# Optimization experiments

Hardware: AMD Instinct MI355X
Metric: run time of the kernel (lower is better)

The kernel has to match this reference:

```python
import jax, jax.numpy as jnp
import numpy as np

D_MODEL, D_STATE, D_CONV, EXPAND = 1024, 16, 4, 2
D_INNER = EXPAND * D_MODEL  # 2048
DT_RANK = (D_MODEL + 15) // 16  # 64
B, L = 2, 2048


def setup_inputs() -> dict:
    key = jax.random.key(0)
    ks = jax.random.split(key, 10)
    x = jax.random.normal(ks[0], (B, L, D_MODEL), dtype=jnp.float32)
    # Linear weights (torch convention: (out, in)); Mamba uses bias=False for in/out proj
    in_proj_w = jax.random.normal(ks[1], (2 * D_INNER, D_MODEL), dtype=jnp.float32) / np.sqrt(D_MODEL)
    conv_w = jax.random.normal(ks[2], (D_INNER, 1, D_CONV), dtype=jnp.float32) / np.sqrt(D_CONV)
    conv_b = jax.random.normal(ks[3], (D_INNER,), dtype=jnp.float32) * 0.02
    x_proj_w = jax.random.normal(ks[4], (DT_RANK + 2 * D_STATE, D_INNER), dtype=jnp.float32) / np.sqrt(D_INNER)
    dt_proj_w = jax.random.normal(ks[5], (D_INNER, DT_RANK), dtype=jnp.float32) * (DT_RANK ** -0.5)
    # dt bias init so softplus(bias) in [dt_min, dt_max]
    dt_min, dt_max = 1e-3, 1e-1
    u = jax.random.uniform(ks[6], (D_INNER,), dtype=jnp.float32)
    dt = jnp.exp(u * (np.log(dt_max) - np.log(dt_min)) + np.log(dt_min))
    dt_proj_b = dt + jnp.log(-jnp.expm1(-dt))  # inverse softplus
    # S4D-real init: A = -(1..d_state)
    A_log = jnp.log(jnp.tile(jnp.arange(1, D_STATE + 1, dtype=jnp.float32), (D_INNER, 1)))
    D_skip = jnp.ones((D_INNER,), dtype=jnp.float32)
    out_proj_w = jax.random.normal(ks[7], (D_MODEL, D_INNER), dtype=jnp.float32) / np.sqrt(D_INNER)
    return {"x": x, "in_proj_w": in_proj_w, "conv_w": conv_w, "conv_b": conv_b,
            "x_proj_w": x_proj_w, "dt_proj_w": dt_proj_w, "dt_proj_b": dt_proj_b,
            "A_log": A_log, "D_skip": D_skip, "out_proj_w": out_proj_w}


def _mamba_forward(x, in_proj_w, conv_w, conv_b, x_proj_w, dt_proj_w, dt_proj_b, A_log, D_skip, out_proj_w):
    Bsz, Lseq, _ = x.shape
    xz = jnp.einsum('bld,ed->ble', x, in_proj_w)          # (B, L, 2*d_inner)
    x_in, z = jnp.split(xz, 2, axis=-1)                    # each (B, L, d_inner)
    # depthwise causal conv1d (left pad d_conv-1)
    xc = jnp.transpose(x_in, (0, 2, 1))                    # (B, d_inner, L)
    xc = jax.lax.conv_general_dilated(
        xc, conv_w, window_strides=(1,), padding=[(D_CONV - 1, 0)],
        dimension_numbers=('NCH', 'OIH', 'NCH'), feature_group_count=D_INNER)
    xc = xc + conv_b[None, :, None]
    x_act = jax.nn.silu(jnp.transpose(xc, (0, 2, 1)))      # (B, L, d_inner)
    # input-dependent SSM parameters
    x_dbl = jnp.einsum('bld,ed->ble', x_act, x_proj_w)     # (B, L, dt_rank+2*d_state)
    dt_low, Bm, Cm = jnp.split(x_dbl, [DT_RANK, DT_RANK + D_STATE], axis=-1)
    delta = jax.nn.softplus(jnp.einsum('blr,dr->bld', dt_low, dt_proj_w) + dt_proj_b)  # (B,L,d)
    A = -jnp.exp(A_log)                                    # (d_inner, d_state)

    def step(h, inp):
        d_t, B_t, C_t, u_t = inp                           # (B,d),(B,N),(B,N),(B,d)
        dA = jnp.exp(d_t[..., None] * A)                   # (B,d,N)
        dBu = (d_t * u_t)[..., None] * B_t[:, None, :]     # (B,d,N)
        h = dA * h + dBu
        y = jnp.einsum('bdn,bn->bd', h, C_t)
        return h, y

    h0 = jnp.zeros((Bsz, D_INNER, D_STATE), dtype=x.dtype)
    xs = (jnp.swapaxes(delta, 0, 1), jnp.swapaxes(Bm, 0, 1),
          jnp.swapaxes(Cm, 0, 1), jnp.swapaxes(x_act, 0, 1))
    _, ys = jax.lax.scan(step, h0, xs)                     # ys: (L, B, d_inner)
    y = jnp.swapaxes(ys, 0, 1) + x_act * D_skip            # skip connection
    y = y * jax.nn.silu(z)                                 # gate
    return jnp.einsum('bld,ed->ble', y, out_proj_w)        # (B, L, d_model)


def reference(x, in_proj_w, conv_w, conv_b, x_proj_w, dt_proj_w, dt_proj_b, A_log, D_skip, out_proj_w):
    return _mamba_forward(x, in_proj_w, conv_w, conv_b, x_proj_w, dt_proj_w, dt_proj_b, A_log, D_skip, out_proj_w)
```

## Files before the change

kernel.cpp:

```cpp
#include <hip/hip_runtime.h>
#include <hip/hip_bf16.h>
#include <cstdint>

#define D_STATE 16
#define D_INNER 2048
#define DT_RANK 64
#define SEQ 2048
#define BL 4096
#define NCHUNK 128
#define CHUNK 16
#define XP_N 96
#define XP_KS 8
#define LOG2E 1.44269504088896340736f

typedef short bf16x8 __attribute__((ext_vector_type(8)));
typedef short short8 __attribute__((ext_vector_type(8)));
typedef float f32x4 __attribute__((ext_vector_type(4)));

__device__ __forceinline__ float siluf(float x) {
  return __fdividef(x, 1.f + __expf(-x));
}

__device__ __forceinline__ float softplusf(float v) {
  return fmaxf(v, 0.f) + __logf(1.f + __expf(-fabsf(v)));
}

__device__ __forceinline__ float exp2fast(float x) {
  return __builtin_amdgcn_exp2f(x);
}

__device__ __forceinline__ unsigned short f2bf_bits(float x) {
  __hip_bfloat16 h = __float2bfloat16(x);
  return *reinterpret_cast<unsigned short*>(&h);
}

__device__ __forceinline__ float bf2f(unsigned short u) {
  return __int_as_float(((unsigned int)u) << 16);
}

__device__ __forceinline__ void gload_lds16(const void* g, void* l) {
  __builtin_amdgcn_global_load_lds((const __attribute__((address_space(1))) unsigned int*)g,
                                   (__attribute__((address_space(3))) unsigned int*)l,
                                   16, 0, 0);
}

#define BARRIER() asm volatile("s_barrier" ::: "memory")
#define VMCNT(n)  asm volatile("s_waitcnt vmcnt(" #n ")" ::: "memory")

__global__ __launch_bounds__(256) void f2bf_multi(const float* __restrict__ x, __hip_bfloat16* __restrict__ x_bf,
                                                  const float* __restrict__ inw, __hip_bfloat16* __restrict__ inw_bf,
                                                  const float* __restrict__ xpw, __hip_bfloat16* __restrict__ wpad,
                                                  const float* __restrict__ dtw, __hip_bfloat16* __restrict__ dtw_bf,
                                                  const float* __restrict__ outw, __hip_bfloat16* __restrict__ outw_bf) {
  const int blk = blockIdx.x;
  const float* src;
  __hip_bfloat16* dst;
  int base;
  if (blk < 2048)      { src = x;    dst = x_bf;    base = blk; }
  else if (blk < 4096) { src = inw;  dst = inw_bf;  base = blk - 2048; }
  else if (blk < 4192) { src = xpw;  dst = wpad;    base = blk - 4096; }
  else if (blk < 4256) { src = dtw;  dst = dtw_bf;  base = blk - 4192; }
  else                 { src = outw; dst = outw_bf; base = blk - 4256; }
  const int i = (base * 256 + threadIdx.x) * 8;
  float4 v0 = *reinterpret_cast<const float4*>(&src[i]);
  float4 v1 = *reinterpret_cast<const float4*>(&src[i + 4]);
  short8 r;
  r[0] = f2bf_bits(v0.x); r[1] = f2bf_bits(v0.y); r[2] = f2bf_bits(v0.z); r[3] = f2bf_bits(v0.w);
  r[4] = f2bf_bits(v1.x); r[5] = f2bf_bits(v1.y); r[6] = f2bf_bits(v1.z); r[7] = f2bf_bits(v1.w);
  *reinterpret_cast<short8*>(&dst[i]) = r;
}

__global__ __launch_bounds__(256) void dtlow_bf_kernel(const float* __restrict__ x_dbl,
                                                       __hip_bfloat16* __restrict__ dtlow_bf) {
  const int i = blockIdx.x * 256 + threadIdx.x;
  const int row = i >> 3;
  const int c8 = (i & 7) * 8;
  float4 v0 = *reinterpret_cast<const float4*>(&x_dbl[(size_t)row * 96 + c8]);
  float4 v1 = *reinterpret_cast<const float4*>(&x_dbl[(size_t)row * 96 + c8 + 4]);
  short8 r;
  r[0] = f2bf_bits(v0.x); r[1] = f2bf_bits(v0.y); r[2] = f2bf_bits(v0.z); r[3] = f2bf_bits(v0.w);
  r[4] = f2bf_bits(v1.x); r[5] = f2bf_bits(v1.y); r[6] = f2bf_bits(v1.z); r[7] = f2bf_bits(v1.w);
  *reinterpret_cast<short8*>(&dtlow_bf[(size_t)row * 64 + c8]) = r;
}

template <typename OutT>
__global__ __launch_bounds__(512, 1) void gemm256_8ph(const __hip_bfloat16* __restrict__ A,
                                                      const __hip_bfloat16* __restrict__ B,
                                                      OutT* __restrict__ C,
                                                      int K, int lda, int ldb, int ldc) {
  __shared__ __align__(16) unsigned short lds[65536];
  const int tid = threadIdx.x;
  const int wv = tid >> 6, lane = tid & 63;
  const int wr = wv >> 2, wc = wv & 3;
  const int m0 = blockIdx.y * 256, n0 = blockIdx.x * 256;
  const int frow = lane & 15;
  const int fu = lane >> 4;
  const int rsw = frow & 7;
  const int sr = lane >> 3;
  const int su = (lane & 7) ^ sr;

  const unsigned short* Ag = (const unsigned short*)A;
  const unsigned short* Bg = (const unsigned short*)B;

  f32x4 acc[8][4];
#pragma unroll
  for (int i = 0; i < 8; ++i)
#pragma unroll
    for (int j = 0; j < 4; ++j) acc[i][j] = {0.f, 0.f, 0.f, 0.f};

  auto stageA = [&](int buf, int g, int kg) {
    const int rowb = g * 64 + wv * 8;
    gload_lds16(&Ag[(size_t)(m0 + rowb + sr) * lda + kg + su * 8],
                &lds[buf * 32768 + rowb * 64]);
  };
  auto stageB = [&](int buf, int g, int kg) {
    const int rowb = g * 64 + wv * 8;
    gload_lds16(&Bg[(size_t)(n0 + rowb + sr) * ldb + kg + su * 8],
                &lds[buf * 32768 + 16384 + rowb * 64]);
  };
  auto fragA = [&](int buf, int mi, int kk) -> bf16x8 {
    const int row = wr * 128 + mi * 16 + frow;
    return *reinterpret_cast<const bf16x8*>(
        &lds[buf * 32768 + row * 64 + (((kk << 2) | fu) ^ rsw) * 8]);
  };
  auto fragB = [&](int buf, int ni, int kk) -> bf16x8 {
    const int row = wc * 64 + ni * 16 + frow;
    return *reinterpret_cast<const bf16x8*>(
        &lds[buf * 32768 + 16384 + row * 64 + (((kk << 2) | fu) ^ rsw) * 8]);
  };

#define QUAD(MB)                                                                        \
  _Pragma("unroll")                                                                     \
  for (int mi = 0; mi < 4; ++mi)                                                        \
    _Pragma("unroll")                                                                   \
    for (int ni = 0; ni < 4; ++ni)                                                      \
      acc[MB + mi][ni] =                                                                \
          __builtin_amdgcn_mfma_f32_16x16x32_bf16(af[mi], bfr[ni], acc[MB + mi][ni], 0, 0, 0);

  stageB(0, 0, 0); stageB(0, 1, 0); stageB(0, 2, 0); stageB(0, 3, 0);
  stageA(0, 0, 0); stageA(0, 2, 0); stageA(0, 1, 0); stageA(0, 3, 0);
  VMCNT(2);
  BARRIER();

  const int NT = K >> 6;
  int cur = 0;
  for (int t = 0; t < NT - 1; ++t) {
    const int nxt = cur ^ 1;
    const int kn = (t + 1) << 6;
    bf16x8 af[4], bfr[4];
#pragma unroll
    for (int mi = 0; mi < 4; ++mi) af[mi] = fragA(cur, mi, 0);
#pragma unroll
    for (int ni = 0; ni < 4; ++ni) bfr[ni] = fragB(cur, ni, 0);
    stageB(nxt, 0, kn); stageB(nxt, 1, kn);
    VMCNT(2);
    BARRIER();
    __builtin_amdgcn_s_setprio(1);
    QUAD(0);
    __builtin_amdgcn_s_setprio(0);
    BARRIER();
#pragma unroll
    for (int mi = 0; mi < 4; ++mi) af[mi] = fragA(cur, 4 + mi, 0);
    stageB(nxt, 2, kn); stageB(nxt, 3, kn);
    BARRIER();
    __builtin_amdgcn_s_setprio(1);
    QUAD(4);
    __builtin_amdgcn_s_setprio(0);
    BARRIER();
#pragma unroll
    for (int mi = 0; mi < 4; ++mi) af[mi] = fragA(cur, mi, 1);
#pragma unroll
    for (int ni = 0; ni < 4; ++ni) bfr[ni] = fragB(cur, ni, 1);
    stageA(nxt, 0, kn); stageA(nxt, 2, kn);
    BARRIER();
    __builtin_amdgcn_s_setprio(1);
    QUAD(0);
    __builtin_amdgcn_s_setprio(0);
    BARRIER();
#pragma unroll
    for (int mi = 0; mi < 4; ++mi) af[mi] = fragA(cur, 4 + mi, 1);
    stageA(nxt, 1, kn); stageA(nxt, 3, kn);
    VMCNT(2);
    BARRIER();
    __builtin_amdgcn_s_setprio(1);
    QUAD(4);
    __builtin_amdgcn_s_setprio(0);
    BARRIER();
    cur = nxt;
  }
  {
    bf16x8 af[4], bfr[4];
#pragma unroll
    for (int mi = 0; mi < 4; ++mi) af[mi] = fragA(cur, mi, 0);
#pragma unroll
    for (int ni = 0; ni < 4; ++ni) bfr[ni] = fragB(cur, ni, 0);
    VMCNT(0);
    BARRIER();
    __builtin_amdgcn_s_setprio(1);
    QUAD(0);
    __builtin_amdgcn_s_setprio(0);
    BARRIER();
#pragma unroll
    for (int mi = 0; mi < 4; ++mi) af[mi] = fragA(cur, 4 + mi, 0);
    BARRIER();
    __builtin_amdgcn_s_setprio(1);
    QUAD(4);
    __builtin_amdgcn_s_setprio(0);
    BARRIER();
#pragma unroll
    for (int mi = 0; mi < 4; ++mi) af[mi] = fragA(cur, mi, 1);
#pragma unroll
    for (int ni = 0; ni < 4; ++ni) bfr[ni] = fragB(cur, ni, 1);
    BARRIER();
    __builtin_amdgcn_s_setprio(1);
    QUAD(0);
    __builtin_amdgcn_s_setprio(0);
    BARRIER();
#pragma unroll
    for (int mi = 0; mi < 4; ++mi) af[mi] = fragA(cur, 4 + mi, 1);
    __builtin_amdgcn_s_setprio(1);
    QUAD(4);
    __builtin_amdgcn_s_setprio(0);
  }
#undef QUAD

  const int crow = fu * 4;
  const int ccol = frow;
#pragma unroll
  for (int mi = 0; mi < 8; ++mi)
#pragma unroll
    for (int ni = 0; ni < 4; ++ni) {
      const int gcol = n0 + wc * 64 + ni * 16 + ccol;
#pragma unroll
      for (int j = 0; j < 4; ++j) {
        const int grow = m0 + wr * 128 + mi * 16 + crow + j;
        if constexpr (sizeof(OutT) == 2) {
          C[(size_t)grow * ldc + gcol] = __float2bfloat16(acc[mi][ni][j]);
        } else {
          C[(size_t)grow * ldc + gcol] = acc[mi][ni][j];
        }
      }
    }
}

template <int BM, int BN>
__device__ __forceinline__ void stage_tiles(const unsigned short* __restrict__ Ag,
                                            const unsigned short* __restrict__ Bg,
                                            unsigned short* buf, int m0, int n0, int k0,
                                            int lda, int ldb, int sr, int sk, int wv) {
#pragma unroll
  for (int g = 0; g < BM / 64; ++g)
    gload_lds16(&Ag[(size_t)(m0 + g * 64 + sr) * lda + k0 + sk], &buf[g * 2048 + wv * 512]);
#pragma unroll
  for (int g = 0; g < BN / 64; ++g)
    gload_lds16(&Bg[(size_t)(n0 + g * 64 + sr) * ldb + k0 + sk], &buf[BM * 32 + g * 2048 + wv * 512]);
}

template <int BM, int BN, int NSTORE, bool SPLITK, typename OutT>
__global__ __launch_bounds__(256) void gemm_bt(const __hip_bfloat16* __restrict__ A,
                                               const __hip_bfloat16* __restrict__ B,
                                               OutT* __restrict__ C,
                                               int K, int lda, int ldb, int ldc) {
  constexpr int WM = BM / 2, WN = BN / 2;
  constexpr int MI = WM / 16, NI = WN / 16;
  constexpr int BUFS = (BM + BN) * 32;
  __shared__ __align__(16) unsigned short lds[2 * BUFS];
  const int tid = threadIdx.x;
  const int wv = tid >> 6, lane = tid & 63;
  const int wr = wv >> 1, wc = wv & 1;
  const int m0 = blockIdx.y * BM;
  int n0, koff;
  if constexpr (SPLITK) {
    n0 = 0;
    koff = blockIdx.x * K;
    C += (size_t)blockIdx.x * BL * NSTORE;
  } else {
    n0 = blockIdx.x * BN;
    koff = 0;
  }
  const int sr = tid >> 2;
  const int sk = (tid & 3) * 8;
  const int frow = lane & 15;
  const int fk = (lane >> 4) * 8;

  f32x4 acc[MI][NI];
#pragma unroll
  for (int i = 0; i < MI; ++i)
#pragma unroll
    for (int j = 0; j < NI; ++j) acc[i][j] = {0.f, 0.f, 0.f, 0.f};

  const unsigned short* Ag = (const unsigned short*)A;
  const unsigned short* Bg = (const unsigned short*)B;

  stage_tiles<BM, BN>(Ag, Bg, &lds[0], m0, n0, koff, lda, ldb, sr, sk, wv);
  __syncthreads();
  int sel = 0;
  for (int k0 = 0; k0 < K; k0 += 32) {
    if (k0 + 32 < K)
      stage_tiles<BM, BN>(Ag, Bg, &lds[(sel ^ 1) * BUFS], m0, n0, koff + k0 + 32, lda, ldb, sr, sk, wv);
    const unsigned short* Abuf = &lds[sel * BUFS];
    const unsigned short* Bbuf = &lds[sel * BUFS + BM * 32];
    bf16x8 af[MI], bfr[NI];
#pragma unroll
    for (int mi = 0; mi < MI; ++mi)
      af[mi] = *reinterpret_cast<const bf16x8*>(&Abuf[(wr * WM + mi * 16 + frow) * 32 + fk]);
#pragma unroll
    for (int ni = 0; ni < NI; ++ni)
      bfr[ni] = *reinterpret_cast<const bf16x8*>(&Bbuf[(wc * WN + ni * 16 + frow) * 32 + fk]);
#pragma unroll
    for (int mi = 0; mi < MI; ++mi)
#pragma unroll
      for (int ni = 0; ni < NI; ++ni)
        acc[mi][ni] = __builtin_amdgcn_mfma_f32_16x16x32_bf16(af[mi], bfr[ni], acc[mi][ni], 0, 0, 0);
    __syncthreads();
    sel ^= 1;
  }

  const int crow = (lane >> 4) * 4;
  const int ccol = lane & 15;
#pragma unroll
  for (int mi = 0; mi < MI; ++mi)
#pragma unroll
    for (int ni = 0; ni < NI; ++ni) {
      const int gcol = n0 + wc * WN + ni * 16 + ccol;
      if constexpr (NSTORE < BN) {
        if (gcol >= NSTORE) continue;
      }
#pragma unroll
      for (int j = 0; j < 4; ++j) {
        const int grow = m0 + wr * WM + mi * 16 + crow + j;
        if constexpr (sizeof(OutT) == 2) {
          C[(size_t)grow * ldc + gcol] = __float2bfloat16(acc[mi][ni][j]);
        } else {
          C[(size_t)grow * ldc + gcol] = acc[mi][ni][j];
        }
      }
    }
}

__global__ __launch_bounds__(256) void xproj_reduce(const float* __restrict__ Cpart,
                                                    float* __restrict__ x_dbl) {
  const int i = blockIdx.x * 256 + threadIdx.x;
  float s = 0.f;
#pragma unroll
  for (int z = 0; z < XP_KS; ++z) s += Cpart[(size_t)z * BL * XP_N + i];
  x_dbl[i] = s;
}

__global__ __launch_bounds__(256) void conv_silu_kernel(const __hip_bfloat16* __restrict__ xz_bf,
                                                        const float* __restrict__ conv_w,
                                                        const float* __restrict__ conv_b,
                                                        __hip_bfloat16* __restrict__ x_act_bf) {
  const int idx = blockIdx.x * 256 + threadIdx.x;
  const int d8 = (idx << 3) & (D_INNER - 1);
  const int bl = idx >> 8;
  const int l = bl & (SEQ - 1);

  float acc[8];
  {
    float4 cb0 = *reinterpret_cast<const float4*>(&conv_b[d8]);
    float4 cb1 = *reinterpret_cast<const float4*>(&conv_b[d8 + 4]);
    acc[0] = cb0.x; acc[1] = cb0.y; acc[2] = cb0.z; acc[3] = cb0.w;
    acc[4] = cb1.x; acc[5] = cb1.y; acc[6] = cb1.z; acc[7] = cb1.w;
  }
  float4 cw[8];
#pragma unroll
  for (int j = 0; j < 8; ++j)
    cw[j] = *reinterpret_cast<const float4*>(&conv_w[(d8 + j) * 4]);

#pragma unroll
  for (int k = 0; k < 4; ++k) {
    if (l + k - 3 >= 0) {
      short8 v = *reinterpret_cast<const short8*>(&xz_bf[(size_t)(bl + k - 3) * 4096 + d8]);
      const float w0[8] = {cw[0].x, cw[1].x, cw[2].x, cw[3].x, cw[4].x, cw[5].x, cw[6].x, cw[7].x};
      const float w1[8] = {cw[0].y, cw[1].y, cw[2].y, cw[3].y, cw[4].y, cw[5].y, cw[6].y, cw[7].y};
      const float w2[8] = {cw[0].z, cw[1].z, cw[2].z, cw[3].z, cw[4].z, cw[5].z, cw[6].z, cw[7].z};
      const float w3[8] = {cw[0].w, cw[1].w, cw[2].w, cw[3].w, cw[4].w, cw[5].w, cw[6].w, cw[7].w};
      const float* wk = (k == 0) ? w0 : (k == 1) ? w1 : (k == 2) ? w2 : w3;
#pragma unroll
      for (int j = 0; j < 8; ++j) acc[j] = fmaf(bf2f((unsigned short)v[j]), wk[j], acc[j]);
    }
  }

  short8 ob;
#pragma unroll
  for (int j = 0; j < 8; ++j) ob[j] = f2bf_bits(siluf(acc[j]));
  *reinterpret_cast<short8*>(&x_act_bf[(size_t)bl * D_INNER + d8]) = ob;
}

__global__ __launch_bounds__(256) void scan_pass1(const __hip_bfloat16* __restrict__ delta_bf,
                                                  const __hip_bfloat16* __restrict__ x_act_bf,
                                                  const float* __restrict__ x_dbl,
                                                  const float* __restrict__ A_log,
                                                  const float* __restrict__ dt_proj_b,
                                                  float* __restrict__ chunkS,
                                                  __hip_bfloat16* __restrict__ chunkH) {
  const int blk = blockIdx.x;
  const int d = ((blk & 7) << 8) + threadIdx.x;
  const int c = (blk >> 3) & (NCHUNK - 1);
  const int b = blk >> 10;
  const int base = b * SEQ + c * CHUNK;

  float Av[16];
#pragma unroll
  for (int q = 0; q < 4; ++q) {
    float4 a = *reinterpret_cast<const float4*>(&A_log[d * 16 + q * 4]);
    Av[q * 4 + 0] = -__expf(a.x) * LOG2E; Av[q * 4 + 1] = -__expf(a.y) * LOG2E;
    Av[q * 4 + 2] = -__expf(a.z) * LOG2E; Av[q * 4 + 3] = -__expf(a.w) * LOG2E;
  }
  const float bias = dt_proj_b[d];

  const unsigned short* dp = (const unsigned short*)delta_bf + (size_t)base * D_INNER + d;
  const unsigned short* up = (const unsigned short*)x_act_bf + (size_t)base * D_INNER + d;
  const float* xb = x_dbl + (size_t)base * 96 + DT_RANK;

  float h[16];
#pragma unroll
  for (int n = 0; n < 16; ++n) h[n] = 0.f;
  float S = 0.f;

  float dv0 = bf2f(dp[0]), uv0 = bf2f(up[0]);
  float dv1 = bf2f(dp[D_INNER]), uv1 = bf2f(up[D_INNER]);
  dp += 2 * D_INNER; up += 2 * D_INNER;
  for (int l = 0; l < CHUNK; ++l) {
    const float dv2 = bf2f(*dp), uv2 = bf2f(*up);
    dp += D_INNER; up += D_INNER;

    const float dv = softplusf(dv0 + bias);
    S += dv;
    const float du = dv * uv0;
#pragma unroll
    for (int n = 0; n < 16; ++n) {
      const float dA = exp2fast(dv * Av[n]);
      h[n] = fmaf(dA, h[n], du * xb[n]);
    }
    xb += 96;
    dv0 = dv1; uv0 = uv1; dv1 = dv2; uv1 = uv2;
  }

  const size_t sidx = (size_t)(b * NCHUNK + c) * D_INNER + d;
  chunkS[sidx] = S;
  unsigned short* hp = (unsigned short*)chunkH + sidx * 16;
  short8 h0v, h1v;
#pragma unroll
  for (int n = 0; n < 8; ++n) { h0v[n] = f2bf_bits(h[n]); h1v[n] = f2bf_bits(h[8 + n]); }
  *reinterpret_cast<short8*>(hp) = h0v;
  *reinterpret_cast<short8*>(hp + 8) = h1v;
}

__global__ __launch_bounds__(256) void scan_pass2(const float* __restrict__ chunkS,
                                                  const float* __restrict__ A_log,
                                                  __hip_bfloat16* chunkH) {
  const int s = blockIdx.x * 256 + threadIdx.x;
  const int n = s & 15;
  const int d = (s >> 4) & (D_INNER - 1);
  const int b = s >> 15;
  const float Aval = -__expf(A_log[d * 16 + n]) * LOG2E;

  unsigned short* hb = (unsigned short*)chunkH;
  size_t sidx = (size_t)b * NCHUNK * D_INNER + d;
  float aS = chunkS[sidx];
  float hE = bf2f(hb[sidx * 16 + n]);
  float H = 0.f;
  for (int c = 0; c < NCHUNK; ++c) {
    const size_t sidx2 = sidx + D_INNER;
    const float naS = chunkS[sidx2];
    const float nhE = bf2f(hb[sidx2 * 16 + n]);
    const float aP = exp2fast(Aval * aS);
    hb[sidx * 16 + n] = f2bf_bits(H);
    H = fmaf(aP, H, hE);
    sidx = sidx2; aS = naS; hE = nhE;
  }
}

__global__ __launch_bounds__(256) void scan_pass3(const __hip_bfloat16* __restrict__ delta_bf,
                                                  const __hip_bfloat16* __restrict__ x_act_bf,
                                                  const float* __restrict__ x_dbl,
                                                  const float* __restrict__ A_log,
                                                  const float* __restrict__ dt_proj_b,
                                                  const __hip_bfloat16* __restrict__ chunkH0,
                                                  const float* __restrict__ D_skip,
                                                  __hip_bfloat16* xz_bf) {
  const int blk = blockIdx.x;
  const int d = ((blk & 7) << 8) + threadIdx.x;
  const int c = (blk >> 3) & (NCHUNK - 1);
  const int b = blk >> 10;
  const int base = b * SEQ + c * CHUNK;

  float Av[16];
#pragma unroll
  for (int q = 0; q < 4; ++q) {
    float4 a = *reinterpret_cast<const float4*>(&A_log[d * 16 + q * 4]);
    Av[q * 4 + 0] = -__expf(a.x) * LOG2E; Av[q * 4 + 1] = -__expf(a.y) * LOG2E;
    Av[q * 4 + 2] = -__expf(a.z) * LOG2E; Av[q * 4 + 3] = -__expf(a.w) * LOG2E;
  }
  const float bias = dt_proj_b[d];
  const float Dv = D_skip[d];

  const unsigned short* dp = (const unsigned short*)delta_bf + (size_t)base * D_INNER + d;
  const unsigned short* up = (const unsigned short*)x_act_bf + (size_t)base * D_INNER + d;
  const float* xb = x_dbl + (size_t)base * 96 + DT_RANK;
  const unsigned short* zr = (const unsigned short*)xz_bf + (size_t)base * 4096 + D_INNER + d;
  __hip_bfloat16* yp = xz_bf + (size_t)base * 4096 + d;

  float h[16];
  {
    const unsigned short* hp = (const unsigned short*)chunkH0 +
                               ((size_t)(b * NCHUNK + c) * D_INNER + d) * 16;
    short8 a8 = *reinterpret_cast<const short8*>(hp);
    short8 b8 = *reinterpret_cast<const short8*>(hp + 8);
#pragma unroll
    for (int n = 0; n < 8; ++n) {
      h[n] = bf2f((unsigned short)a8[n]);
      h[8 + n] = bf2f((unsigned short)b8[n]);
    }
  }

  float dv0 = bf2f(dp[0]), uv0 = bf2f(up[0]);
  float dv1 = bf2f(dp[D_INNER]), uv1 = bf2f(up[D_INNER]);
  dp += 2 * D_INNER; up += 2 * D_INNER;
  float zv = bf2f(zr[0]);
  zr += 4096;
  for (int l = 0; l < CHUNK; ++l) {
    const float dv2 = bf2f(*dp), uv2 = bf2f(*up);
    dp += D_INNER; up += D_INNER;
    const float nzv = bf2f(*zr);
    zr += 4096;

    const float dv = softplusf(dv0 + bias);
    const float du = dv * uv0;
    float p = 0.f;
#pragma unroll
    for (int n = 0; n < 16; ++n) {
      const float dA = exp2fast(dv * Av[n]);
      h[n] = fmaf(dA, h[n], du * xb[n]);
      p = fmaf(h[n], xb[16 + n], p);
    }
    xb += 96;
    const float yv = fmaf(uv0, Dv, p) * siluf(zv);
    yp[0] = __float2bfloat16(yv);
    yp += 4096;

    dv0 = dv1; uv0 = uv1; dv1 = dv2; uv1 = uv2; zv = nzv;
  }
}

extern "C" void kernel_launch(void* const* d_in, const int* in_sizes, int n_in,
                              void* d_out, int out_size, void* d_ws, size_t ws_size,
                              hipStream_t stream) {
  const float* x          = (const float*)d_in[0];
  const float* in_proj_w  = (const float*)d_in[1];
  const float* conv_w     = (const float*)d_in[2];
  const float* conv_b     = (const float*)d_in[3];
  const float* x_proj_w   = (const float*)d_in[4];
  const float* dt_proj_w  = (const float*)d_in[5];
  const float* dt_proj_b  = (const float*)d_in[6];
  const float* A_log      = (const float*)d_in[7];
  const float* D_skip     = (const float*)d_in[8];
  const float* out_proj_w = (const float*)d_in[9];
  float* out = (float*)d_out;

  char* ws = (char*)d_ws;
  __hip_bfloat16* xz_bf    = (__hip_bfloat16*)(ws);
  __hip_bfloat16* x_act_bf = (__hip_bfloat16*)(ws + 33554432);
  __hip_bfloat16* delta_bf = (__hip_bfloat16*)(ws + 50331648);
  __hip_bfloat16* x_bf     = (__hip_bfloat16*)(ws + 67108864);
  __hip_bfloat16* inw_bf   = (__hip_bfloat16*)(ws + 75497472);
  float* Cpart             = (float*)(ws + 67108864);
  float* x_dbl             = (float*)(ws + 100663296);
  __hip_bfloat16* chunkH   = (__hip_bfloat16*)(ws + 102236160);
  float* chunkS            = (float*)(ws + 135790592);
  __hip_bfloat16* wpad     = (__hip_bfloat16*)(ws + 137887744);
  __hip_bfloat16* dtlow_bf = (__hip_bfloat16*)(ws + 138412032);
  __hip_bfloat16* dtw_bf   = (__hip_bfloat16*)(ws + 138936320);
  __hip_bfloat16* outw_bf  = (__hip_bfloat16*)(ws + 139198464);

  f2bf_multi<<<5280, 256, 0, stream>>>(x, x_bf, in_proj_w, inw_bf, x_proj_w, wpad,
                                       dt_proj_w, dtw_bf, out_proj_w, outw_bf);

  gemm256_8ph<__hip_bfloat16><<<dim3(16, 16), 512, 0, stream>>>(
      x_bf, inw_bf, xz_bf, 1024, 1024, 1024, 4096);

  conv_silu_kernel<<<(BL * D_INNER) / 8 / 256, 256, 0, stream>>>(
      xz_bf, conv_w, conv_b, x_act_bf);

  gemm_bt<128, 128, XP_N, true, float><<<dim3(XP_KS, 32), 256, 0, stream>>>(
      x_act_bf, wpad, Cpart, 2048 / XP_KS, 2048, 2048, XP_N);
  xproj_reduce<<<(BL * XP_N) / 256, 256, 0, stream>>>(Cpart, x_dbl);

  dtlow_bf_kernel<<<128, 256, 0, stream>>>(x_dbl, dtlow_bf);
  gemm_bt<128, 128, 128, false, __hip_bfloat16><<<dim3(16, 32), 256, 0, stream>>>(
      dtlow_bf, dtw_bf, delta_bf, 64, 64, 64, 2048);

  scan_pass1<<<2048, 256, 0, stream>>>(delta_bf, x_act_bf, x_dbl, A_log, dt_proj_b,
                                       chunkS, chunkH);
  scan_pass2<<<256, 256, 0, stream>>>(chunkS, A_log, chunkH);
  scan_pass3<<<2048, 256, 0, stream>>>(delta_bf, x_act_bf, x_dbl, A_log, dt_proj_b,
                                       chunkH, D_skip, xz_bf);

  gemm_bt<128, 64, 64, false, float><<<dim3(16, 32), 256, 0, stream>>>(
      xz_bf, outw_bf, out, 2048, 4096, 2048, 1024);
}
```

Baseline: 212.2 us.

## Swizzle GEMM blocks across XCDs, fuse dtlow cast, prefetch scan_pass2 deeper

Remaps workgroup IDs in the in_proj, dt_proj and out_proj GEMMs so that blocks landing on the same XCD cover neighbouring tiles, aiming at better L2 reuse. Folds the bf16 conversion of the dt_low columns into the x_proj split-K reduction kernel, removing one launch and one pass over x_dbl. Restructures the serial chunk-carry loop in scan_pass2 to keep four chunks of loads in flight, hiding memory latency. The cost is extra integer index arithmetic and a few more registers.

Result: faster. 207.3 us (median of 2 runs) (-2.3%).

```diff
diff --git a/kernel.cpp b/kernel.cpp
--- a/kernel.cpp
+++ b/kernel.cpp
@@ -70,19 +70,6 @@
   *reinterpret_cast<short8*>(&dst[i]) = r;
 }
 
-__global__ __launch_bounds__(256) void dtlow_bf_kernel(const float* __restrict__ x_dbl,
-                                                       __hip_bfloat16* __restrict__ dtlow_bf) {
-  const int i = blockIdx.x * 256 + threadIdx.x;
-  const int row = i >> 3;
-  const int c8 = (i & 7) * 8;
-  float4 v0 = *reinterpret_cast<const float4*>(&x_dbl[(size_t)row * 96 + c8]);
-  float4 v1 = *reinterpret_cast<const float4*>(&x_dbl[(size_t)row * 96 + c8 + 4]);
-  short8 r;
-  r[0] = f2bf_bits(v0.x); r[1] = f2bf_bits(v0.y); r[2] = f2bf_bits(v0.z); r[3] = f2bf_bits(v0.w);
-  r[4] = f2bf_bits(v1.x); r[5] = f2bf_bits(v1.y); r[6] = f2bf_bits(v1.z); r[7] = f2bf_bits(v1.w);
-  *reinterpret_cast<short8*>(&dtlow_bf[(size_t)row * 64 + c8]) = r;
-}
-
 template <typename OutT>
 __global__ __launch_bounds__(512, 1) void gemm256_8ph(const __hip_bfloat16* __restrict__ A,
                                                       const __hip_bfloat16* __restrict__ B,
@@ -92,7 +79,10 @@
   const int tid = threadIdx.x;
   const int wv = tid >> 6, lane = tid & 63;
   const int wr = wv >> 2, wc = wv & 3;
-  const int m0 = blockIdx.y * 256, n0 = blockIdx.x * 256;
+  const int nwg = gridDim.x * gridDim.y;
+  const int bid = blockIdx.y * gridDim.x + blockIdx.x;
+  const int swz = (bid & 7) * (nwg >> 3) + (bid >> 3);
+  const int m0 = (swz / gridDim.x) * 256, n0 = (swz % gridDim.x) * 256;
   const int frow = lane & 15;
   const int fu = lane >> 4;
   const int rsw = frow & 7;
@@ -256,7 +246,7 @@
     gload_lds16(&Bg[(size_t)(n0 + g * 64 + sr) * ldb + k0 + sk], &buf[BM * 32 + g * 2048 + wv * 512]);
 }
 
-template <int BM, int BN, int NSTORE, bool SPLITK, typename OutT>
+template <int BM, int BN, int NSTORE, bool SPLITK, bool XSWZ, typename OutT>
 __global__ __launch_bounds__(256) void gemm_bt(const __hip_bfloat16* __restrict__ A,
                                                const __hip_bfloat16* __restrict__ B,
                                                OutT* __restrict__ C,
@@ -268,13 +258,21 @@
   const int tid = threadIdx.x;
   const int wv = tid >> 6, lane = tid & 63;
   const int wr = wv >> 1, wc = wv & 1;
-  const int m0 = blockIdx.y * BM;
-  int n0, koff;
+  int m0, n0, koff;
   if constexpr (SPLITK) {
+    m0 = blockIdx.y * BM;
     n0 = 0;
     koff = blockIdx.x * K;
     C += (size_t)blockIdx.x * BL * NSTORE;
+  } else if constexpr (XSWZ) {
+    const int nwg = gridDim.x * gridDim.y;
+    const int bid = blockIdx.y * gridDim.x + blockIdx.x;
+    const int swz = (bid & 7) * (nwg >> 3) + (bid >> 3);
+    m0 = (swz / gridDim.x) * BM;
+    n0 = (swz % gridDim.x) * BN;
+    koff = 0;
   } else {
+    m0 = blockIdx.y * BM;
     n0 = blockIdx.x * BN;
     koff = 0;
   }
@@ -339,12 +337,16 @@
 }
 
 __global__ __launch_bounds__(256) void xproj_reduce(const float* __restrict__ Cpart,
-                                                    float* __restrict__ x_dbl) {
+                                                    float* __restrict__ x_dbl,
+                                                    __hip_bfloat16* __restrict__ dtlow_bf) {
   const int i = blockIdx.x * 256 + threadIdx.x;
   float s = 0.f;
 #pragma unroll
   for (int z = 0; z < XP_KS; ++z) s += Cpart[(size_t)z * BL * XP_N + i];
   x_dbl[i] = s;
+  const int row = i / XP_N;
+  const int col = i - row * XP_N;
+  if (col < DT_RANK) dtlow_bf[(size_t)row * DT_RANK + col] = __float2bfloat16(s);
 }
 
 __global__ __launch_bounds__(256) void conv_silu_kernel(const __hip_bfloat16* __restrict__ xz_bf,
@@ -458,18 +460,27 @@
   const float Aval = -__expf(A_log[d * 16 + n]) * LOG2E;
 
   unsigned short* hb = (unsigned short*)chunkH;
-  size_t sidx = (size_t)b * NCHUNK * D_INNER + d;
-  float aS = chunkS[sidx];
-  float hE = bf2f(hb[sidx * 16 + n]);
+  size_t s0 = (size_t)b * NCHUNK * D_INNER + d;
+  float aSq[4], hEq[4];
+#pragma unroll
+  for (int j = 0; j < 4; ++j) {
+    aSq[j] = chunkS[s0 + (size_t)j * D_INNER];
+    hEq[j] = bf2f(hb[(s0 + (size_t)j * D_INNER) * 16 + n]);
+  }
   float H = 0.f;
-  for (int c = 0; c < NCHUNK; ++c) {
-    const size_t sidx2 = sidx + D_INNER;
-    const float naS = chunkS[sidx2];
-    const float nhE = bf2f(hb[sidx2 * 16 + n]);
-    const float aP = exp2fast(Aval * aS);
-    hb[sidx * 16 + n] = f2bf_bits(H);
-    H = fmaf(aP, H, hE);
-    sidx = sidx2; aS = naS; hE = nhE;
+  for (int c = 0; c < NCHUNK; c += 4) {
+#pragma unroll
+    for (int j = 0; j < 4; ++j) {
+      const size_t scur = s0 + (size_t)j * D_INNER;
+      const size_t snext = scur + 4 * (size_t)D_INNER;
+      const float naS = chunkS[snext];
+      const float nhE = bf2f(hb[snext * 16 + n]);
+      const float aP = exp2fast(Aval * aSq[j]);
+      hb[scur * 16 + n] = f2bf_bits(H);
+      H = fmaf(aP, H, hEq[j]);
+      aSq[j] = naS; hEq[j] = nhE;
+    }
+    s0 += 4 * (size_t)D_INNER;
   }
 }
 
@@ -584,12 +595,11 @@
   conv_silu_kernel<<<(BL * D_INNER) / 8 / 256, 256, 0, stream>>>(
       xz_bf, conv_w, conv_b, x_act_bf);
 
-  gemm_bt<128, 128, XP_N, true, float><<<dim3(XP_KS, 32), 256, 0, stream>>>(
+  gemm_bt<128, 128, XP_N, true, false, float><<<dim3(XP_KS, 32), 256, 0, stream>>>(
       x_act_bf, wpad, Cpart, 2048 / XP_KS, 2048, 2048, XP_N);
-  xproj_reduce<<<(BL * XP_N) / 256, 256, 0, stream>>>(Cpart, x_dbl);
-
-  dtlow_bf_kernel<<<128, 256, 0, stream>>>(x_dbl, dtlow_bf);
-  gemm_bt<128, 128, 128, false, __hip_bfloat16><<<dim3(16, 32), 256, 0, stream>>>(
+  xproj_reduce<<<(BL * XP_N) / 256, 256, 0, stream>>>(Cpart, x_dbl, dtlow_bf);
+
+  gemm_bt<128, 128, 128, false, true, __hip_bfloat16><<<dim3(16, 32), 256, 0, stream>>>(
       dtlow_bf, dtw_bf, delta_bf, 64, 64, 64, 2048);
 
   scan_pass1<<<2048, 256, 0, stream>>>(delta_bf, x_act_bf, x_dbl, A_log, dt_proj_b,
@@ -598,6 +608,6 @@
   scan_pass3<<<2048, 256, 0, stream>>>(delta_bf, x_act_bf, x_dbl, A_log, dt_proj_b,
                                        chunkH, D_skip, xz_bf);
 
-  gemm_bt<128, 64, 64, false, float><<<dim3(16, 32), 256, 0, stream>>>(
+  gemm_bt<128, 64, 64, false, true, float><<<dim3(16, 32), 256, 0, stream>>>(
       xz_bf, outw_bf, out, 2048, 4096, 2048, 1024);
 }
```
